# Kernel tuning notes

Hardware: AMD Instinct MI355X
Metric: run time of the kernel (lower is better)

## Reference

```python
import jax, jax.numpy as jnp
import numpy as np

B, S, D = 4, 2048, 1024
H = 16
HD = D // H


def setup_inputs() -> dict:
    key = jax.random.key(0)
    ks = jax.random.split(key, 6)
    s = 1.0 / np.sqrt(D)
    x = jax.random.normal(ks[0], (B, S, D), dtype=jnp.float32)
    Wq = jax.random.uniform(ks[1], (D, D), jnp.float32, -s, s)
    Wk = jax.random.uniform(ks[2], (D, D), jnp.float32, -s, s)
    Wv = jax.random.uniform(ks[3], (D, D), jnp.float32, -s, s)
    Wo = jax.random.uniform(ks[4], (D, D), jnp.float32, -s, s)
    bo = jax.random.uniform(ks[5], (D,), jnp.float32, -s, s)
    return {"x": x, "Wq": Wq, "Wk": Wk, "Wv": Wv, "Wo": Wo, "bo": bo}


def reference(x, Wq, Wk, Wv, Wo, bo):
    b, n, _ = x.shape
    # QKV projections (nn.Linear applies x @ W.T; W here stored as [d_in, d_out])
    q = (x @ Wq).reshape(b, n, H, HD).transpose(0, 2, 1, 3)  # [b,h,s,hd]
    k = (x @ Wk).reshape(b, n, H, HD).transpose(0, 2, 1, 3)
    v = (x @ Wv).reshape(b, n, H, HD).transpose(0, 2, 1, 3)
    scores = jnp.einsum('bhqd,bhkd->bhqk', q, k) / np.sqrt(HD).astype(np.float32)
    causal = jnp.tril(jnp.ones((n, n), dtype=bool))  # True = keep
    scores = jnp.where(causal, scores, -jnp.inf)
    attn = jax.nn.softmax(scores, axis=-1)
    ctx = jnp.einsum('bhqk,bhkd->bhqd', attn, v)  # [b,h,s,hd]
    ctx = ctx.transpose(0, 2, 1, 3).reshape(b, n, D)
    return ctx @ Wo + bo
```

## Files before the change

kernel.cpp:

```cpp
#include <hip/hip_runtime.h>

#define NB 4
#define NS 2048
#define ND 1024
#define NH 16
#define NHD 64
#define NTOK (NB*NS)

typedef float f32x4 __attribute__((ext_vector_type(4)));
typedef __bf16 bf16x8 __attribute__((ext_vector_type(8)));
typedef __bf16 bf16x4 __attribute__((ext_vector_type(4)));

#define MFMA16(a,b,c) __builtin_amdgcn_mfma_f32_16x16x32_bf16((a),(b),(c),0,0,0)
#define SBAR() __builtin_amdgcn_s_barrier()
#define VMCNT(n) asm volatile("s_waitcnt vmcnt(" #n ")" ::: "memory")
#define LGKM(n) asm volatile("s_waitcnt lgkmcnt(" #n ")" ::: "memory")
#define SCHEDB() __builtin_amdgcn_sched_barrier(0)

__device__ __forceinline__ float fexp2(float x) {
#if __has_builtin(__builtin_amdgcn_exp2f)
  return __builtin_amdgcn_exp2f(x);
#else
  return __expf(x * 0.69314718056f);
#endif
}

__device__ __forceinline__ void gload_lds16(const __bf16* g, const __bf16* l) {
  __builtin_amdgcn_global_load_lds(
      (const __attribute__((address_space(1))) void*)(uintptr_t)(const void*)g,
      (__attribute__((address_space(3))) void*)(uint32_t)(uintptr_t)(const void*)l,
      16, 0, 0);
}

__global__ void k_prep(const float* __restrict__ x,
                       const float* __restrict__ w0, const float* __restrict__ w1,
                       const float* __restrict__ w2, const float* __restrict__ w3,
                       __bf16* __restrict__ xb, __bf16* __restrict__ wqkvt,
                       __bf16* __restrict__ wot) {
  __shared__ float tl[64][65];
  const int bi = blockIdx.x;
  if (bi < 1024) {
    const int z = bi >> 8, rem = bi & 255;
    const float* src = (z==0)?w0:(z==1)?w1:(z==2)?w2:w3;
    __bf16* dst = (z<3) ? (wqkvt + (size_t)z*ND*ND) : wot;
    const int kb = (rem>>4)*64, nb = (rem&15)*64;
    const int c = threadIdx.x & 63, r0 = threadIdx.x >> 6;
    for (int i=0;i<16;i++) { int r = r0*16+i; tl[r][c] = src[(size_t)(kb+r)*ND + nb + c]; }
    __syncthreads();
    for (int i=0;i<16;i++) { int r = r0*16+i; dst[(size_t)(nb+r)*ND + kb + c] = (__bf16)tl[c][r]; }
  } else {
    const int i = (bi - 1024)*256 + threadIdx.x;
    float4 v = ((const float4*)x)[i];
    bf16x4 o = { (__bf16)v.x, (__bf16)v.y, (__bf16)v.z, (__bf16)v.w };
    ((bf16x4*)xb)[i] = o;
  }
}

__global__ __launch_bounds__(256, 2) void k_gemm_qkv(
    const __bf16* __restrict__ A, const __bf16* __restrict__ Bt,
    __bf16* __restrict__ qs, __bf16* __restrict__ ks, __bf16* __restrict__ vt) {
  constexpr int BUFE = (256+128)*32;
  __shared__ __align__(16) __bf16 lds[3*BUFE];
  const int tid = threadIdx.x;
  const int wid = tid>>6, lane = tid&63;
  const int wr = wid>>1, wc = wid&1;
  const int lrow = lane&15, lg = lane>>4;
  const int srow4 = lane>>2;
  const int scol  = ((lane&3) ^ ((lane>>3)&3))*8;

  const int id  = blockIdx.x;
  const int xcd = id & 7;
  const int nl  = id >> 3;
  const int st  = nl >> 5;
  const int u   = nl & 31;
  const int bx  = xcd*4 + (u >> 3);
  const int by  = st*8 + (u & 7);
  const int m0 = bx*256, n0 = by*128;

  auto stage = [&](int t, int bsel) {
    __bf16* buf = lds + bsel*BUFE;
    const int k0 = t*32;
    #pragma unroll
    for (int i=0;i<4;i++) {
      int c = wid + i*4;
      gload_lds16(A + (size_t)(m0 + c*16 + srow4)*ND + k0 + scol, buf + c*512);
    }
    #pragma unroll
    for (int i=0;i<2;i++) {
      int c = wid + i*4;
      gload_lds16(Bt + (size_t)(n0 + c*16 + srow4)*ND + k0 + scol, buf + 8192 + c*512);
    }
  };

  const int slot = (lg ^ ((lrow>>1)&3)) << 4;
  const int abase = (wr*128 + lrow)*64 + slot;
  const int bbase = 16384 + (wc*64 + lrow)*64 + slot;

  f32x4 acc[8][4];
  f32x4 zero = {0.f,0.f,0.f,0.f};
  #pragma unroll
  for (int i=0;i<8;i++) for (int j=0;j<4;j++) acc[i][j] = zero;

  stage(0,0);
  stage(1,1);
  for (int t=0; t<32; ++t) {
    if (t < 30) stage(t+2, (t+2)%3);
    if (t < 30)      { VMCNT(12); }
    else if (t == 30){ VMCNT(6);  }
    else             { VMCNT(0);  }
    SBAR();
    const char* L = (const char*)(lds + (t%3)*BUFE);
    bf16x8 bfr[4], af[8];
    #pragma unroll
    for (int cb=0;cb<4;cb++) bfr[cb] = *(const bf16x8*)(L + bbase + cb*1024);
    #pragma unroll
    for (int mf=0;mf<4;mf++) af[mf] = *(const bf16x8*)(L + abase + mf*1024);
    SCHEDB();
    #pragma unroll
    for (int mf=4;mf<8;mf++) af[mf] = *(const bf16x8*)(L + abase + mf*1024);
    LGKM(4);
    SCHEDB();
    __builtin_amdgcn_s_setprio(1);
    #pragma unroll
    for (int mf=0;mf<4;mf++)
      #pragma unroll
      for (int cb=0;cb<4;cb++)
        acc[mf][cb] = MFMA16(af[mf], bfr[cb], acc[mf][cb]);
    __builtin_amdgcn_s_setprio(0);
    LGKM(0);
    SCHEDB();
    __builtin_amdgcn_s_setprio(1);
    #pragma unroll
    for (int mf=4;mf<8;mf++)
      #pragma unroll
      for (int cb=0;cb<4;cb++)
        acc[mf][cb] = MFMA16(af[mf], bfr[cb], acc[mf][cb]);
    __builtin_amdgcn_s_setprio(0);
    SBAR();
  }

  const int which = by >> 3;
  const int h = (by&7)*2 + wc;
  __bf16* ws = lds + wid*8192;
  const int tokbase = m0 + wr*128;
  const int b = tokbase >> 11, s0 = tokbase & 2047;

  if (which < 2) {
    __bf16* dst = which ? ks : qs;
    #pragma unroll
    for (int mf=0;mf<8;mf++)
      #pragma unroll
      for (int cb=0;cb<4;cb++)
        #pragma unroll
        for (int r=0;r<4;r++) {
          int row = mf*16 + lg*4 + r;
          int chunk = (cb*2 + (lrow>>3)) ^ (row&7);
          *(__bf16*)((char*)ws + row*128 + chunk*16 + (lrow&7)*2) = (__bf16)acc[mf][cb][r];
        }
    #pragma unroll
    for (int p=0;p<16;p++) {
      int row = p*8 + (lane>>3);
      int chunk = (lane&7) ^ (row&7);
      bf16x8 v = *(const bf16x8*)((char*)ws + row*128 + chunk*16);
      *(bf16x8*)(dst + ((size_t)(b*NH + h)*NS + s0 + row)*NHD + (lane&7)*8) = v;
    }
  } else {
    #pragma unroll
    for (int mf=0;mf<8;mf++)
      #pragma unroll
      for (int cb=0;cb<4;cb++) {
        bf16x4 pk = { (__bf16)acc[mf][cb][0], (__bf16)acc[mf][cb][1],
                      (__bf16)acc[mf][cb][2], (__bf16)acc[mf][cb][3] };
        int hd = cb*16 + lrow;
        int slotv = (mf*2 + (lg>>1)) ^ (hd&15);
        *(bf16x4*)((char*)ws + hd*256 + slotv*16 + (lg&1)*8) = pk;
      }
    #pragma unroll
    for (int p=0;p<16;p++) {
      int idx = p*64 + lane;
      int hd = idx>>4, c = idx&15;
      bf16x8 v = *(const bf16x8*)((char*)ws + hd*256 + ((c ^ (hd&15)))*16);
      *(bf16x8*)(vt + ((size_t)(b*NH + h)*NHD + hd)*NS + s0 + c*8) = v;
    }
  }
}

__global__ __launch_bounds__(512, 2) void k_gemm_out(
    const __bf16* __restrict__ A, const __bf16* __restrict__ Bt,
    const float* __restrict__ bo, float* __restrict__ out) {
  constexpr int BUFE = (256+128)*64;
  __shared__ __align__(16) __bf16 lds[3*BUFE];
  const int tid = threadIdx.x;
  const int wid = tid>>6, lane = tid&63;
  const int wr = wid>>1, wc = wid&1;
  const int lrow = lane&15, lg = lane>>4;
  const int srow = lane>>3;
  const int scol = ((lane&7) ^ srow)*8;

  const int id  = blockIdx.x;
  const int xcd = id & 7;
  const int nl  = id >> 3;
  const int bx  = xcd*4 + (nl >> 3);
  const int by  = nl & 7;
  const int m0 = bx*256, n0 = by*128;

  auto stage = [&](int t, int bsel) {
    __bf16* buf = lds + bsel*BUFE;
    const int k0 = t*64;
    #pragma unroll
    for (int i=0;i<4;i++) {
      int c = wid + i*8;
      gload_lds16(A + (size_t)(m0 + c*8 + srow)*ND + k0 + scol, buf + c*512);
    }
    #pragma unroll
    for (int i=0;i<2;i++) {
      int c = wid + i*8;
      gload_lds16(Bt + (size_t)(n0 + c*8 + srow)*ND + k0 + scol, buf + 16384 + c*512);
    }
  };

  int kx[8];
  #pragma unroll
  for (int kk=0;kk<8;kk++) kx[kk] = ((kk ^ (lrow&7)) << 4);
  const int abase = (wr*64 + lrow)*128;
  const int bbase = 32768 + (wc*64 + lrow)*128;

  f32x4 acc[4][4];
  f32x4 zero = {0.f,0.f,0.f,0.f};
  #pragma unroll
  for (int i=0;i<4;i++) for (int j=0;j<4;j++) acc[i][j] = zero;

  stage(0,0);
  stage(1,1);
  for (int t=0; t<16; ++t) {
    if (t < 14) stage(t+2, (t+2)%3);
    if (t < 14)      { VMCNT(12); }
    else if (t == 14){ VMCNT(6);  }
    else             { VMCNT(0);  }
    SBAR();
    const char* L = (const char*)(lds + (t%3)*BUFE);
    bf16x8 bfr[4][2], af[4][2];
    #pragma unroll
    for (int cb=0;cb<4;cb++)
      #pragma unroll
      for (int ksi=0;ksi<2;ksi++)
        bfr[cb][ksi] = *(const bf16x8*)(L + bbase + cb*2048 + kx[ksi*4+lg]);
    #pragma unroll
    for (int mf=0;mf<2;mf++)
      #pragma unroll
      for (int ksi=0;ksi<2;ksi++)
        af[mf][ksi] = *(const bf16x8*)(L + abase + mf*2048 + kx[ksi*4+lg]);
    SCHEDB();
    #pragma unroll
    for (int mf=2;mf<4;mf++)
      #pragma unroll
      for (int ksi=0;ksi<2;ksi++)
        af[mf][ksi] = *(const bf16x8*)(L + abase + mf*2048 + kx[ksi*4+lg]);
    LGKM(4);
    SCHEDB();
    __builtin_amdgcn_s_setprio(1);
    #pragma unroll
    for (int mf=0;mf<2;mf++)
      #pragma unroll
      for (int cb=0;cb<4;cb++)
        #pragma unroll
        for (int ksi=0;ksi<2;ksi++)
          acc[mf][cb] = MFMA16(af[mf][ksi], bfr[cb][ksi], acc[mf][cb]);
    __builtin_amdgcn_s_setprio(0);
    LGKM(0);
    SCHEDB();
    __builtin_amdgcn_s_setprio(1);
    #pragma unroll
    for (int mf=2;mf<4;mf++)
      #pragma unroll
      for (int cb=0;cb<4;cb++)
        #pragma unroll
        for (int ksi=0;ksi<2;ksi++)
          acc[mf][cb] = MFMA16(af[mf][ksi], bfr[cb][ksi], acc[mf][cb]);
    __builtin_amdgcn_s_setprio(0);
    SBAR();
  }

  #pragma unroll
  for (int cb=0;cb<4;cb++) {
    const int n = n0 + wc*64 + cb*16 + lrow;
    const float bias = bo[n];
    #pragma unroll
    for (int mf=0;mf<4;mf++)
      #pragma unroll
      for (int r=0;r<4;r++) {
        const int m = m0 + wr*64 + mf*16 + lg*4 + r;
        out[(size_t)m*ND + n] = acc[mf][cb][r] + bias;
      }
  }
}

__global__ __launch_bounds__(256, 3) void k_attn(
    const __bf16* __restrict__ qs, const __bf16* __restrict__ ks,
    const __bf16* __restrict__ vt, __bf16* __restrict__ ctx) {
  __shared__ __align__(16) __bf16 sK[2][64*64];
  __shared__ __align__(16) __bf16 sV[2][64*64];
  __shared__ __align__(16) __bf16 sP[4][32*72];
  const int tid = threadIdx.x, w = tid >> 6, lane = tid & 63;
  const int lrow = lane & 15, lg = lane >> 4;
  const int bh = blockIdx.x;
  const int bq = 15 - blockIdx.y;
  const int nt = 2*bq + 2;
  const size_t base = (size_t)bh * NS * NHD;
  const __bf16* Kg = ks + base;
  const __bf16* Vg = vt + base;
  __bf16* sPw = sP[w];

  const int q0w = bq*128 + w*32;
  bf16x8 qf[2][2];
  for (int rb=0;rb<2;rb++)
    for (int kk=0;kk<2;kk++) {
      bf16x8 v = *(const bf16x8*)(qs + base + (size_t)(q0w + rb*16 + lrow)*NHD + kk*32 + lg*8);
      bf16x8 o;
      for (int j=0;j<8;j++) o[j] = (__bf16)((float)v[j] * 0.1803368801f);
      qf[rb][kk] = o;
    }

  int koffB[4][2];
  for (int cb=0;cb<4;cb++) {
    int r = cb*16 + lrow;
    for (int kk=0;kk<2;kk++)
      koffB[cb][kk] = r*128 + (((kk*4 + lg) ^ (r & 7)) << 4);
  }
  const int s_r[2]  = { (w + 0)*8 + (lane>>3), (w + 4)*8 + (lane>>3) };
  const int s_u[2]  = { (lane&7) ^ (s_r[0]&7), (lane&7) ^ (s_r[1]&7) };

  f32x4 zero = {0.f,0.f,0.f,0.f};
  f32x4 oacc[2][4];
  float psum[2] = {0.f, 0.f};
  for (int rb=0;rb<2;rb++) for(int cb=0;cb<4;cb++) oacc[rb][cb]=zero;

  for (int i=0;i<2;i++) {
    gload_lds16(Kg + (size_t)s_r[i]*NHD + s_u[i]*8,              sK[0] + (w + i*4)*512);
    gload_lds16(Vg + (size_t)s_r[i]*NS  + s_u[i]*8,              sV[0] + (w + i*4)*512);
  }
  asm volatile("s_waitcnt vmcnt(0)" ::: "memory");
  __syncthreads();

  int buf = 0;
  for (int t = 0; t < nt; ++t) {
    if (t+1 < nt) {
      const __bf16* Kt = Kg + (size_t)(t+1)*64*NHD;
      for (int i=0;i<2;i++) {
        gload_lds16(Kt + (size_t)s_r[i]*NHD + s_u[i]*8,          sK[buf^1] + (w + i*4)*512);
        gload_lds16(Vg + (size_t)s_r[i]*NS + (t+1)*64 + s_u[i]*8, sV[buf^1] + (w + i*4)*512);
      }
    }
    if (!(t == nt-1 && w < 2)) {
      const __bf16* bK = sK[buf];
      const __bf16* bV = sV[buf];
      const bool bdry = (t >= nt-2);
      for (int cb=0;cb<4;cb++) {
        bf16x8 kf0 = *(const bf16x8*)((const char*)bK + koffB[cb][0]);
        bf16x8 kf1 = *(const bf16x8*)((const char*)bK + koffB[cb][1]);
        const int kvb = t*64 + cb*16 + lg*4;
        for (int rb=0;rb<2;rb++) {
          f32x4 s4 = MFMA16(kf0, qf[rb][0], zero);
          s4 = MFMA16(kf1, qf[rb][1], s4);
          const int qg = q0w + rb*16 + lrow;
          float e0 = fexp2(s4[0]), e1 = fexp2(s4[1]);
          float e2 = fexp2(s4[2]), e3 = fexp2(s4[3]);
          if (bdry) {
            if (kvb + 0 > qg) e0 = 0.f;
            if (kvb + 1 > qg) e1 = 0.f;
            if (kvb + 2 > qg) e2 = 0.f;
            if (kvb + 3 > qg) e3 = 0.f;
          }
          psum[rb] += (e0 + e1) + (e2 + e3);
          bf16x4 pk = { (__bf16)e0, (__bf16)e1, (__bf16)e2, (__bf16)e3 };
          *(bf16x4*)(sPw + (rb*16 + lrow)*72 + cb*16 + lg*4) = pk;
        }
      }
      for (int kk=0;kk<2;kk++) {
        bf16x8 pa0 = *(const bf16x8*)(sPw + (lrow)*72      + kk*32 + lg*8);
        bf16x8 pa1 = *(const bf16x8*)(sPw + (16 + lrow)*72 + kk*32 + lg*8);
        for (int cb=0;cb<4;cb++) {
          bf16x8 vb = *(const bf16x8*)((const char*)bV + koffB[cb][kk]);
          oacc[0][cb] = MFMA16(pa0, vb, oacc[0][cb]);
          oacc[1][cb] = MFMA16(pa1, vb, oacc[1][cb]);
        }
      }
    }
    asm volatile("s_waitcnt vmcnt(0)" ::: "memory");
    __syncthreads();
    buf ^= 1;
  }

  float inv[2];
  for (int rb=0;rb<2;rb++) {
    float s = psum[rb];
    s += __shfl_xor(s, 16);
    s += __shfl_xor(s, 32);
    inv[rb] = 1.0f / s;
  }

  __bf16* ws = &sK[0][0] + w*2048;
  const int b = bh >> 4, h = bh & 15;
  for (int rb=0;rb<2;rb++)
    for (int cb=0;cb<4;cb++)
      for (int r=0;r<4;r++) {
        int row = rb*16 + lg*4 + r;
        float nrm = __shfl(inv[rb], lg*4 + r);
        int chunk = (cb*2 + (lrow>>3)) ^ (row&7);
        *(__bf16*)((char*)ws + row*128 + chunk*16 + (lrow&7)*2) =
            (__bf16)(oacc[rb][cb][r] * nrm);
      }
  for (int p=0;p<4;p++) {
    int row = p*8 + (lane>>3);
    int chunk = (lane&7) ^ (row&7);
    bf16x8 v = *(const bf16x8*)((char*)ws + row*128 + chunk*16);
    int q = q0w + row;
    *(bf16x8*)(ctx + ((size_t)(b*NS + q))*ND + h*NHD + (lane&7)*8) = v;
  }
}

extern "C" void kernel_launch(void* const* d_in, const int* in_sizes, int n_in,
                              void* d_out, int out_size, void* d_ws, size_t ws_size,
                              hipStream_t stream) {
  const float* x  = (const float*)d_in[0];
  const float* Wq = (const float*)d_in[1];
  const float* Wk = (const float*)d_in[2];
  const float* Wv = (const float*)d_in[3];
  const float* Wo = (const float*)d_in[4];
  const float* bo = (const float*)d_in[5];
  float* out = (float*)d_out;

  __bf16* xb    = (__bf16*)d_ws;
  __bf16* wqkvt = xb    + (size_t)NTOK*ND;
  __bf16* wot   = wqkvt + (size_t)3*ND*ND;
  __bf16* qsc   = wot   + (size_t)ND*ND;
  __bf16* ksc   = qsc   + (size_t)NTOK*ND;
  __bf16* vtc   = ksc   + (size_t)NTOK*ND;
  __bf16* ctx   = vtc   + (size_t)NTOK*ND;

  k_prep<<<1024 + NTOK*ND/(4*256), 256, 0, stream>>>(x, Wq, Wk, Wv, Wo, xb, wqkvt, wot);
  k_gemm_qkv<<<768, 256, 0, stream>>>(xb, wqkvt, qsc, ksc, vtc);
  k_attn<<<dim3(NB*NH, NS/128), 256, 0, stream>>>(qsc, ksc, vtc, ctx);
  k_gemm_out<<<256, 512, 0, stream>>>(ctx, wot, bo, out);
}
```

Baseline: 143.3 us.

## Enlarge attention query tile to 256 rows with 8 waves sharing K/V loads

The attention kernel now uses 512-thread blocks covering 256 query rows, with each of 8 waves owning 32 rows. All waves share one double-buffered K/V tile in LDS, so each K/V tile is loaded once for twice as many queries, halving global K/V traffic. Block ordering is changed to interleave long and short causal tiles for load balance. The trade-off is more waves idling on the causal boundary tiles, since waves whose rows lie below a tile skip it, and fewer blocks in the grid.

```diff
diff --git a/kernel.cpp b/kernel.cpp
--- a/kernel.cpp
+++ b/kernel.cpp
@@ -295,23 +295,23 @@
   }
 }
 
-__global__ __launch_bounds__(256, 3) void k_attn(
+__global__ __launch_bounds__(512, 4) void k_attn(
     const __bf16* __restrict__ qs, const __bf16* __restrict__ ks,
     const __bf16* __restrict__ vt, __bf16* __restrict__ ctx) {
-  __shared__ __align__(16) __bf16 sK[2][64*64];
-  __shared__ __align__(16) __bf16 sV[2][64*64];
-  __shared__ __align__(16) __bf16 sP[4][32*72];
+  __shared__ __align__(16) __bf16 sKV[4][64*64];
+  __shared__ __align__(16) __bf16 sP[8][32*72];
   const int tid = threadIdx.x, w = tid >> 6, lane = tid & 63;
   const int lrow = lane & 15, lg = lane >> 4;
   const int bh = blockIdx.x;
-  const int bq = 15 - blockIdx.y;
-  const int nt = 2*bq + 2;
+  const int y = blockIdx.y;
+  const int bq = (y < 4) ? 7 - y : y - 4;
+  const int nt = 4*bq + 4;
   const size_t base = (size_t)bh * NS * NHD;
   const __bf16* Kg = ks + base;
   const __bf16* Vg = vt + base;
   __bf16* sPw = sP[w];
 
-  const int q0w = bq*128 + w*32;
+  const int q0w = bq*256 + w*32;
   bf16x8 qf[2][2];
   for (int rb=0;rb<2;rb++)
     for (int kk=0;kk<2;kk++) {
@@ -327,34 +327,29 @@
     for (int kk=0;kk<2;kk++)
       koffB[cb][kk] = r*128 + (((kk*4 + lg) ^ (r & 7)) << 4);
   }
-  const int s_r[2]  = { (w + 0)*8 + (lane>>3), (w + 4)*8 + (lane>>3) };
-  const int s_u[2]  = { (lane&7) ^ (s_r[0]&7), (lane&7) ^ (s_r[1]&7) };
+  const int s_r = w*8 + (lane>>3);
+  const int s_u = (lane&7) ^ (s_r&7);
 
   f32x4 zero = {0.f,0.f,0.f,0.f};
   f32x4 oacc[2][4];
   float psum[2] = {0.f, 0.f};
   for (int rb=0;rb<2;rb++) for(int cb=0;cb<4;cb++) oacc[rb][cb]=zero;
 
-  for (int i=0;i<2;i++) {
-    gload_lds16(Kg + (size_t)s_r[i]*NHD + s_u[i]*8,              sK[0] + (w + i*4)*512);
-    gload_lds16(Vg + (size_t)s_r[i]*NS  + s_u[i]*8,              sV[0] + (w + i*4)*512);
-  }
+  gload_lds16(Kg + (size_t)s_r*NHD + s_u*8, sKV[0] + w*512);
+  gload_lds16(Vg + (size_t)s_r*NS  + s_u*8, sKV[2] + w*512);
   asm volatile("s_waitcnt vmcnt(0)" ::: "memory");
   __syncthreads();
 
   int buf = 0;
   for (int t = 0; t < nt; ++t) {
     if (t+1 < nt) {
-      const __bf16* Kt = Kg + (size_t)(t+1)*64*NHD;
-      for (int i=0;i<2;i++) {
-        gload_lds16(Kt + (size_t)s_r[i]*NHD + s_u[i]*8,          sK[buf^1] + (w + i*4)*512);
-        gload_lds16(Vg + (size_t)s_r[i]*NS + (t+1)*64 + s_u[i]*8, sV[buf^1] + (w + i*4)*512);
-      }
-    }
-    if (!(t == nt-1 && w < 2)) {
-      const __bf16* bK = sK[buf];
-      const __bf16* bV = sV[buf];
-      const bool bdry = (t >= nt-2);
+      gload_lds16(Kg + (size_t)((t+1)*64 + s_r)*NHD + s_u*8, sKV[buf^1]     + w*512);
+      gload_lds16(Vg + (size_t)s_r*NS + (t+1)*64 + s_u*8,    sKV[2+(buf^1)] + w*512);
+    }
+    if (t*64 <= q0w + 31) {
+      const __bf16* bK = sKV[buf];
+      const __bf16* bV = sKV[2+buf];
+      const bool bdry = (t*64 + 63 > q0w);
       for (int cb=0;cb<4;cb++) {
         bf16x8 kf0 = *(const bf16x8*)((const char*)bK + koffB[cb][0]);
         bf16x8 kf1 = *(const bf16x8*)((const char*)bK + koffB[cb][1]);
@@ -399,7 +394,7 @@
     inv[rb] = 1.0f / s;
   }
 
-  __bf16* ws = &sK[0][0] + w*2048;
+  __bf16* ws = &sKV[0][0] + w*2048;
   const int b = bh >> 4, h = bh & 15;
   for (int rb=0;rb<2;rb++)
     for (int cb=0;cb<4;cb++)
@@ -440,6 +435,6 @@
 
   k_prep<<<1024 + NTOK*ND/(4*256), 256, 0, stream>>>(x, Wq, Wk, Wv, Wo, xb, wqkvt, wot);
   k_gemm_qkv<<<768, 256, 0, stream>>>(xb, wqkvt, qsc, ksc, vtc);
-  k_attn<<<dim3(NB*NH, NS/128), 256, 0, stream>>>(qsc, ksc, vtc, ctx);
+  k_attn<<<dim3(NB*NH, 8), 512, 0, stream>>>(qsc, ksc, vtc, ctx);
   k_gemm_out<<<256, 512, 0, stream>>>(ctx, wot, bo, out);
 }
```

Measured after the change: 151.8 us. 1.06x slower.
